# Kernel tuning notes

Measured on AMD Instinct MI355X. Metric: run time of the kernel, lower is better.

The kernel has to match this reference:

```python
import jax, jax.numpy as jnp
import numpy as np

N_NODES = 50000
N_EDGES = 1600000
HID = 256
NODE_F = 2
EDGE_F = 7
NUM_LAYERS = 3
EPS = 0.0  # GINEConv default eps


def _glorot(key, shape):
    fan_in, fan_out = shape[0], shape[1]
    lim = float(np.sqrt(6.0 / (fan_in + fan_out)))
    return jax.random.uniform(key, shape, jnp.float32, -lim, lim)


def setup_inputs() -> dict:
    key = jax.random.key(0)
    ks = jax.random.split(key, 16)
    x = jax.random.normal(ks[0], (N_NODES, NODE_F), jnp.float32)
    edge_index = jax.random.randint(ks[1], (2, N_EDGES), 0, N_NODES, jnp.int64)
    edge_attr = jax.random.normal(ks[2], (N_EDGES, EDGE_F), jnp.float32)
    # conv1: lin_edge1 (7->2), nn1 Linear(2->HID)
    We1 = _glorot(ks[3], (EDGE_F, NODE_F)); be1 = jnp.zeros((NODE_F,), jnp.float32)
    W1 = _glorot(ks[4], (NODE_F, HID));     b1 = jnp.zeros((HID,), jnp.float32)
    # conv2: lin_edge2 (7->HID), nn2 Linear(HID->HID)
    We2 = _glorot(ks[5], (EDGE_F, HID));    be2 = jnp.zeros((HID,), jnp.float32)
    W2 = _glorot(ks[6], (HID, HID));        b2 = jnp.zeros((HID,), jnp.float32)
    # endLinear HID->1
    Wend = _glorot(ks[7], (HID, 1));        bend = jnp.zeros((1,), jnp.float32)
    return dict(x=x, edge_index=edge_index, edge_attr=edge_attr,
                We1=We1, be1=be1, W1=W1, b1=b1,
                We2=We2, be2=be2, W2=W2, b2=b2,
                Wend=Wend, bend=bend)


def _gine_conv(h, src, dst, edge_emb, W, b):
    # message: relu(h[src] + lin_edge(edge_attr)); aggregate: scatter-sum at dst
    msg = jax.nn.relu(h[src] + edge_emb)                      # [E, C]
    aggr = jax.ops.segment_sum(msg, dst, num_segments=N_NODES)  # [N, C]
    return ((1.0 + EPS) * h + aggr) @ W + b                   # nn(...)


def reference(x, edge_index, edge_attr, We1, be1, W1, b1, We2, be2, W2, b2, Wend, bend):
    src, dst = edge_index[0], edge_index[1]
    # layer 1
    h = _gine_conv(x, src, dst, edge_attr @ We1 + be1, W1, b1)
    # layers 2..num_layers (shared conv2 weights, batchnorm disabled)
    edge_emb2 = edge_attr @ We2 + be2
    for _ in range(NUM_LAYERS - 1):
        h = jax.nn.relu(h)
        h = _gine_conv(h, src, dst, edge_emb2, W2, b2)
    h = jax.nn.relu(h)
    return jax.nn.sigmoid(h @ Wend + bend)  # [N, 1]
```

## Files before the change

kernel.cpp:

```cpp
#include <hip/hip_runtime.h>
#include <hip/hip_fp16.h>
#include <math.h>

#define N_NODES 50000
#define N_EDGES 1600000
#define HID 256
#define SCAN_B 196

typedef _Float16 f16x8 __attribute__((ext_vector_type(8)));
typedef float f32x4 __attribute__((ext_vector_type(4)));
typedef float v2f __attribute__((ext_vector_type(2)));

static __device__ __forceinline__ __half2 pk_max2(__half2 a, __half2 b) {
    unsigned au = *reinterpret_cast<unsigned*>(&a);
    unsigned bu = *reinterpret_cast<unsigned*>(&b);
    unsigned r;
    asm("v_pk_max_f16 %0, %1, %2" : "=v"(r) : "v"(au), "v"(bu));
    return *reinterpret_cast<__half2*>(&r);
}

static __device__ __forceinline__ unsigned h2u(float lo, float hi) {
    __half2 t = __floats2half2_rn(lo, hi);
    return *reinterpret_cast<unsigned*>(&t);
}

#define PKFMA_LO(ACC, ATTR, W)                                           \
    asm("v_pk_fma_f16 %0, %1, %2, %0 op_sel:[0,0,0] op_sel_hi:[0,1,1]"   \
        : "+v"(ACC) : "v"(ATTR), "v"(W))
#define PKFMA_HI(ACC, ATTR, W)                                           \
    asm("v_pk_fma_f16 %0, %1, %2, %0 op_sel:[1,0,0] op_sel_hi:[1,1,1]"   \
        : "+v"(ACC) : "v"(ATTR), "v"(W))

static __device__ __forceinline__ unsigned pack4_fp8(float a, float b, float c, float d) {
    int v = __builtin_amdgcn_cvt_pk_fp8_f32(a, b, 0, false);
    v = __builtin_amdgcn_cvt_pk_fp8_f32(c, d, v, true);
    return (unsigned)v;
}

__global__ __launch_bounds__(256) void hist_kernel(const int* __restrict__ dst,
                                                   int* __restrict__ deg) {
    const int T = gridDim.x * 256;
    const int t = blockIdx.x * 256 + threadIdx.x;
#pragma unroll
    for (int i = 0; i < 4; ++i) {
        int e = t + i * T;
        if (e < N_EDGES) atomicAdd(&deg[dst[e]], 1);
    }
}

__global__ __launch_bounds__(256) void scan1_kernel(const int* __restrict__ deg,
                                                    int* __restrict__ bsum) {
    int idx = blockIdx.x * 256 + threadIdx.x;
    int v = (idx < N_NODES) ? deg[idx] : 0;
#pragma unroll
    for (int off = 32; off > 0; off >>= 1) v += __shfl_down(v, off);
    __shared__ int ws[4];
    if ((threadIdx.x & 63) == 0) ws[threadIdx.x >> 6] = v;
    __syncthreads();
    if (threadIdx.x == 0) bsum[blockIdx.x] = ws[0] + ws[1] + ws[2] + ws[3];
}

__global__ __launch_bounds__(256) void scan2_kernel(int* __restrict__ bsum) {
    __shared__ int s[256];
    int t = threadIdx.x;
    int v = (t < SCAN_B) ? bsum[t] : 0;
    s[t] = v;
    __syncthreads();
    for (int off = 1; off < 256; off <<= 1) {
        int u = (t >= off) ? s[t - off] : 0;
        __syncthreads();
        s[t] += u;
        __syncthreads();
    }
    if (t < SCAN_B) bsum[t] = s[t] - v;
}

__global__ __launch_bounds__(256) void scan3_kernel(const int* __restrict__ deg,
                                                    const int* __restrict__ bsum,
                                                    int* __restrict__ base,
                                                    int* __restrict__ cursor) {
    __shared__ int s[256];
    int t = threadIdx.x;
    int idx = blockIdx.x * 256 + t;
    int v = (idx < N_NODES) ? deg[idx] : 0;
    s[t] = v;
    __syncthreads();
    for (int off = 1; off < 256; off <<= 1) {
        int u = (t >= off) ? s[t - off] : 0;
        __syncthreads();
        s[t] += u;
        __syncthreads();
    }
    if (idx < N_NODES) {
        int bv = bsum[blockIdx.x] + s[t] - v;
        base[idx] = bv;
        cursor[idx] = bv;
    }
    if (idx == 0) base[N_NODES] = N_EDGES;
}

static __device__ __forceinline__ void write_rec(float* __restrict__ rec, int pos,
                                                 const float* __restrict__ ep, int s) {
    float4 v;
    *(__half2*)&v.x = __floats2half2_rn(ep[0], ep[1]);
    *(__half2*)&v.y = __floats2half2_rn(ep[2], ep[3]);
    *(__half2*)&v.z = __floats2half2_rn(ep[4], ep[5]);
    unsigned w = (unsigned)__half_as_ushort(__float2half_rn(ep[6])) |
                 ((unsigned)s << 16);
    v.w = __uint_as_float(w);
    *(float4*)(rec + (size_t)pos * 4) = v;
}

__global__ __launch_bounds__(256) void scatter_rec_kernel(
        const int* __restrict__ src,
        const int* __restrict__ dst,
        const float* __restrict__ ea,
        int* __restrict__ cursor,
        float* __restrict__ rec) {
    const int T = gridDim.x * 256;
    const int t = blockIdx.x * 256 + threadIdx.x;
    const int e0 = t, e1 = t + T, e2 = t + 2 * T, e3 = t + 3 * T;
    const bool v3 = (e3 < N_EDGES);
    int d0 = dst[e0], d1 = dst[e1], d2 = dst[e2];
    int s0 = src[e0], s1 = src[e1], s2 = src[e2];
    int d3 = v3 ? dst[e3] : 0;
    int s3 = v3 ? src[e3] : 0;
    int p0 = atomicAdd(&cursor[d0], 1);
    int p1 = atomicAdd(&cursor[d1], 1);
    int p2 = atomicAdd(&cursor[d2], 1);
    int p3 = v3 ? atomicAdd(&cursor[d3], 1) : 0;
    write_rec(rec, p0, ea + (size_t)e0 * 7, s0);
    write_rec(rec, p1, ea + (size_t)e1 * 7, s1);
    write_rec(rec, p2, ea + (size_t)e2 * 7, s2);
    if (v3) write_rec(rec, p3, ea + (size_t)e3 * 7, s3);
}

__global__ __launch_bounds__(256) void layer1_kernel(
        const float* __restrict__ x,
        const float* __restrict__ rec,
        const int* __restrict__ base,
        const float* __restrict__ We1,
        const float* __restrict__ be1,
        const float* __restrict__ W1,
        const float* __restrict__ b1,
        unsigned* __restrict__ h8) {
    const int lane = threadIdx.x & 63;
    const int wid = threadIdx.x >> 6;
    const int n = blockIdx.x * 4 + wid;
    if (n >= N_NODES) return;
    float w00 = We1[0],  w01 = We1[1],  w10 = We1[2],  w11 = We1[3];
    float w20 = We1[4],  w21 = We1[5],  w30 = We1[6],  w31 = We1[7];
    float w40 = We1[8],  w41 = We1[9],  w50 = We1[10], w51 = We1[11];
    float w60 = We1[12], w61 = We1[13];
    float bb0 = be1[0], bb1 = be1[1];
    float m0 = 0.f, m1 = 0.f;
    const int s0 = base[n], s1 = base[n + 1];
    for (int pos = s0 + lane; pos < s1; pos += 64) {
        float4 a = *(const float4*)(rec + (size_t)pos * 4);
        __half2 hx = *(__half2*)&a.x;
        __half2 hy = *(__half2*)&a.y;
        __half2 hz = *(__half2*)&a.z;
        __half2 hw = *(__half2*)&a.w;
        unsigned uw = __float_as_uint(a.w);
        int s = (int)(uw >> 16);
        float a0 = __low2float(hx),  a1 = __high2float(hx);
        float a2 = __low2float(hy),  a3 = __high2float(hy);
        float a4 = __low2float(hz),  a5 = __high2float(hz);
        float a6 = __low2float(hw);
        float t0 = bb0, t1 = bb1;
        t0 = fmaf(a0, w00, t0); t1 = fmaf(a0, w01, t1);
        t0 = fmaf(a1, w10, t0); t1 = fmaf(a1, w11, t1);
        t0 = fmaf(a2, w20, t0); t1 = fmaf(a2, w21, t1);
        t0 = fmaf(a3, w30, t0); t1 = fmaf(a3, w31, t1);
        t0 = fmaf(a4, w40, t0); t1 = fmaf(a4, w41, t1);
        t0 = fmaf(a5, w50, t0); t1 = fmaf(a5, w51, t1);
        t0 = fmaf(a6, w60, t0); t1 = fmaf(a6, w61, t1);
        float2 xv = *(const float2*)&x[(size_t)s * 2];
        m0 += fmaxf(t0 + xv.x, 0.f);
        m1 += fmaxf(t1 + xv.y, 0.f);
    }
#pragma unroll
    for (int off = 32; off > 0; off >>= 1) {
        m0 += __shfl_down(m0, off);
        m1 += __shfl_down(m1, off);
    }
    m0 = __shfl(m0, 0);
    m1 = __shfl(m1, 0);
    const float t0 = x[n * 2 + 0] + m0;
    const float t1 = x[n * 2 + 1] + m1;
    const int c = lane * 4;
    float4 wa = *(const float4*)&W1[c];
    float4 wb = *(const float4*)&W1[256 + c];
    float4 bv = *(const float4*)&b1[c];
    float4 r;
    r.x = fmaxf(fmaf(t0, wa.x, fmaf(t1, wb.x, bv.x)), 0.f);
    r.y = fmaxf(fmaf(t0, wa.y, fmaf(t1, wb.y, bv.y)), 0.f);
    r.z = fmaxf(fmaf(t0, wa.z, fmaf(t1, wb.z, bv.z)), 0.f);
    r.w = fmaxf(fmaf(t0, wa.w, fmaf(t1, wb.w, bv.w)), 0.f);
    h8[(size_t)n * 64 + lane] = pack4_fp8(r.x, r.y, r.z, r.w);
}

#define EDGEH(RA, HU)                                                  \
    do {                                                               \
        unsigned _ux = __float_as_uint(RA.x);                          \
        unsigned _uy = __float_as_uint(RA.y);                          \
        unsigned _uz = __float_as_uint(RA.z);                          \
        unsigned _uw = __float_as_uint(RA.w);                          \
        unsigned _m0 = bb01u, _m1 = bb23u;                             \
        PKFMA_LO(_m0, _ux, w0au); PKFMA_LO(_m1, _ux, w0bu);            \
        PKFMA_HI(_m0, _ux, w1au); PKFMA_HI(_m1, _ux, w1bu);            \
        PKFMA_LO(_m0, _uy, w2au); PKFMA_LO(_m1, _uy, w2bu);            \
        PKFMA_HI(_m0, _uy, w3au); PKFMA_HI(_m1, _uy, w3bu);            \
        PKFMA_LO(_m0, _uz, w4au); PKFMA_LO(_m1, _uz, w4bu);            \
        PKFMA_HI(_m0, _uz, w5au); PKFMA_HI(_m1, _uz, w5bu);            \
        PKFMA_LO(_m0, _uw, w6au); PKFMA_LO(_m1, _uw, w6bu);            \
        v2f _hf0 = __builtin_amdgcn_cvt_pk_f32_fp8((int)(HU), false);  \
        v2f _hf1 = __builtin_amdgcn_cvt_pk_f32_fp8((int)(HU), true);   \
        __half2 _h0 = __float22half2_rn(make_float2(_hf0.x, _hf0.y));  \
        __half2 _h1 = __float22half2_rn(make_float2(_hf1.x, _hf1.y));  \
        __half2 _m0h = *reinterpret_cast<__half2*>(&_m0);              \
        __half2 _m1h = *reinterpret_cast<__half2*>(&_m1);              \
        _m0h = pk_max2(__hadd2(_m0h, _h0), z2);                        \
        _m1h = pk_max2(__hadd2(_m1h, _h1), z2);                        \
        acc0 = __hadd2(acc0, _m0h);                                    \
        acc1 = __hadd2(acc1, _m1h);                                    \
    } while (0)

#define HLOAD(RA) (h8[(size_t)((unsigned)__builtin_amdgcn_readfirstlane(       \
                       __float_as_int(RA.w)) >> 16) * 64 + lane])

#define LOADG(A0, A1, A2, A3, H0, H1, H2, H3, G)                       \
    do {                                                               \
        const float4* _p = rp + (size_t)(G) * 4;                       \
        A0 = _p[0]; A1 = _p[1]; A2 = _p[2]; A3 = _p[3];                \
        H0 = HLOAD(A0); H1 = HLOAD(A1);                                \
        H2 = HLOAD(A2); H3 = HLOAD(A3);                                \
    } while (0)

#define CONS4(A0, A1, A2, A3, H0, H1, H2, H3)                          \
    do {                                                               \
        EDGEH(A0, H0); EDGEH(A1, H1);                                  \
        EDGEH(A2, H2); EDGEH(A3, H3);                                  \
    } while (0)

__global__ __launch_bounds__(256) void aggr2_kernel(
        const unsigned* __restrict__ h8,
        const float* __restrict__ rec,
        const int* __restrict__ base,
        const float* __restrict__ We2,
        const float* __restrict__ be2,
        __half* __restrict__ accum) {
    const int lane = threadIdx.x & 63;
    const int n = blockIdx.x * 4 + (threadIdx.x >> 6);
    if (n >= N_NODES) return;
    const int c4 = lane * 4;
    const unsigned w0au = h2u(We2[0 * HID + c4], We2[0 * HID + c4 + 1]);
    const unsigned w0bu = h2u(We2[0 * HID + c4 + 2], We2[0 * HID + c4 + 3]);
    const unsigned w1au = h2u(We2[1 * HID + c4], We2[1 * HID + c4 + 1]);
    const unsigned w1bu = h2u(We2[1 * HID + c4 + 2], We2[1 * HID + c4 + 3]);
    const unsigned w2au = h2u(We2[2 * HID + c4], We2[2 * HID + c4 + 1]);
    const unsigned w2bu = h2u(We2[2 * HID + c4 + 2], We2[2 * HID + c4 + 3]);
    const unsigned w3au = h2u(We2[3 * HID + c4], We2[3 * HID + c4 + 1]);
    const unsigned w3bu = h2u(We2[3 * HID + c4 + 2], We2[3 * HID + c4 + 3]);
    const unsigned w4au = h2u(We2[4 * HID + c4], We2[4 * HID + c4 + 1]);
    const unsigned w4bu = h2u(We2[4 * HID + c4 + 2], We2[4 * HID + c4 + 3]);
    const unsigned w5au = h2u(We2[5 * HID + c4], We2[5 * HID + c4 + 1]);
    const unsigned w5bu = h2u(We2[5 * HID + c4 + 2], We2[5 * HID + c4 + 3]);
    const unsigned w6au = h2u(We2[6 * HID + c4], We2[6 * HID + c4 + 1]);
    const unsigned w6bu = h2u(We2[6 * HID + c4 + 2], We2[6 * HID + c4 + 3]);
    const unsigned bb01u = h2u(be2[c4], be2[c4 + 1]);
    const unsigned bb23u = h2u(be2[c4 + 2], be2[c4 + 3]);
    const __half2 z2 = __float2half2_rn(0.f);

    __half2 acc0, acc1;
    {
        unsigned hv = h8[(size_t)n * 64 + lane];
        v2f f0 = __builtin_amdgcn_cvt_pk_f32_fp8((int)hv, false);
        v2f f1 = __builtin_amdgcn_cvt_pk_f32_fp8((int)hv, true);
        acc0 = __float22half2_rn(make_float2(f0.x, f0.y));
        acc1 = __float22half2_rn(make_float2(f1.x, f1.y));
    }
    const int s0 = __builtin_amdgcn_readfirstlane(base[n]);
    const int deg = __builtin_amdgcn_readfirstlane(base[n + 1]) - s0;
    const float4* rp = (const float4*)rec + (size_t)s0;
    const int ng = deg >> 2;

    float4 r0, r1, r2, r3;
    unsigned rh0, rh1, rh2, rh3;
    float4 t0, t1, t2, t3;
    unsigned th0, th1, th2, th3;

    if (ng > 0) {
        LOADG(r0, r1, r2, r3, rh0, rh1, rh2, rh3, 0);
        int g = 1;
        for (; g + 1 < ng; g += 2) {
            LOADG(t0, t1, t2, t3, th0, th1, th2, th3, g);
            CONS4(r0, r1, r2, r3, rh0, rh1, rh2, rh3);
            LOADG(r0, r1, r2, r3, rh0, rh1, rh2, rh3, g + 1);
            CONS4(t0, t1, t2, t3, th0, th1, th2, th3);
        }
        if (g < ng) {
            LOADG(t0, t1, t2, t3, th0, th1, th2, th3, g);
            CONS4(r0, r1, r2, r3, rh0, rh1, rh2, rh3);
            CONS4(t0, t1, t2, t3, th0, th1, th2, th3);
        } else {
            CONS4(r0, r1, r2, r3, rh0, rh1, rh2, rh3);
        }
    }
    for (int i = ng * 4; i < deg; ++i) {
        float4 ra = rp[(size_t)i];
        unsigned hv = HLOAD(ra);
        EDGEH(ra, hv);
    }
    float2 of;
    *(__half2*)&of.x = acc0;
    *(__half2*)&of.y = acc1;
    *(float2*)&accum[(size_t)n * HID + c4] = of;
}

__global__ __launch_bounds__(256) void w2_swizzle_kernel(const float* __restrict__ W,
                                                         __half* __restrict__ W2s) {
    int t = blockIdx.x * 256 + threadIdx.x;
    if (t >= 16 * 8 * 64) return;
    int lane = t & 63;
    int kc = (t >> 6) & 7;
    int ct = t >> 9;
    int k0 = kc * 32 + (lane >> 4) * 8;
    int col = ct * 16 + (lane & 15);
#pragma unroll
    for (int j = 0; j < 8; ++j)
        W2s[(size_t)t * 8 + j] = __float2half(W[(size_t)(k0 + j) * HID + col]);
}

template <bool FUSE_END>
__global__ __launch_bounds__(256) void node2_mfma_kernel(
        const __half* __restrict__ A,
        const __half* __restrict__ W2s,
        const float* __restrict__ b,
        unsigned char* __restrict__ h8,
        const float* __restrict__ Wend,
        const float* __restrict__ bend,
        float* __restrict__ out) {
    const int lane = threadIdx.x & 63;
    const int wv = threadIdx.x >> 6;
    const int n_base = blockIdx.x * 64 + wv * 16;
    if (n_base >= N_NODES) return;
    const int quad = lane >> 4;
    const int mrow = lane & 15;
    f16x8 af[8];
    const __half* ap = A + (size_t)(n_base + mrow) * HID + quad * 8;
#pragma unroll
    for (int kc = 0; kc < 8; ++kc)
        af[kc] = *(const f16x8*)(ap + kc * 32);
    float p0 = 0.f, p1 = 0.f, p2 = 0.f, p3 = 0.f;
#pragma unroll
    for (int ct = 0; ct < 16; ++ct) {
        f32x4 c = {0.f, 0.f, 0.f, 0.f};
        const f16x8* bp = (const f16x8*)W2s + (size_t)(ct * 8) * 64 + lane;
#pragma unroll
        for (int kc = 0; kc < 8; ++kc)
            c = __builtin_amdgcn_mfma_f32_16x16x32_f16(af[kc], bp[(size_t)kc * 64],
                                                       c, 0, 0, 0);
        const int col = ct * 16 + mrow;
        const float bias = b[col];
        if (!FUSE_END) {
#pragma unroll
            for (int r = 0; r < 4; ++r) {
                int n = n_base + quad * 4 + r;
                float v = fmaxf(c[r] + bias, 0.f);
                int pk = __builtin_amdgcn_cvt_pk_fp8_f32(v, v, 0, false);
                if (n < N_NODES)
                    h8[(size_t)n * HID + col] = (unsigned char)(pk & 0xff);
            }
        } else {
            const float we = Wend[col];
            p0 = fmaf(fmaxf(c[0] + bias, 0.f), we, p0);
            p1 = fmaf(fmaxf(c[1] + bias, 0.f), we, p1);
            p2 = fmaf(fmaxf(c[2] + bias, 0.f), we, p2);
            p3 = fmaf(fmaxf(c[3] + bias, 0.f), we, p3);
        }
    }
    if (FUSE_END) {
#pragma unroll
        for (int mask = 1; mask < 16; mask <<= 1) {
            p0 += __shfl_xor(p0, mask);
            p1 += __shfl_xor(p1, mask);
            p2 += __shfl_xor(p2, mask);
            p3 += __shfl_xor(p3, mask);
        }
        if (mrow == 0) {
            const float bd = bend[0];
            int n = n_base + quad * 4;
            if (n + 0 < N_NODES) out[n + 0] = 1.f / (1.f + expf(-(p0 + bd)));
            if (n + 1 < N_NODES) out[n + 1] = 1.f / (1.f + expf(-(p1 + bd)));
            if (n + 2 < N_NODES) out[n + 2] = 1.f / (1.f + expf(-(p2 + bd)));
            if (n + 3 < N_NODES) out[n + 3] = 1.f / (1.f + expf(-(p3 + bd)));
        }
    }
}

extern "C" void kernel_launch(void* const* d_in, const int* in_sizes, int n_in,
                              void* d_out, int out_size, void* d_ws, size_t ws_size,
                              hipStream_t stream) {
    const float* x    = (const float*)d_in[0];
    const int*   ei   = (const int*)d_in[1];
    const float* ea   = (const float*)d_in[2];
    const float* We1  = (const float*)d_in[3];
    const float* be1  = (const float*)d_in[4];
    const float* W1   = (const float*)d_in[5];
    const float* b1   = (const float*)d_in[6];
    const float* We2  = (const float*)d_in[7];
    const float* be2  = (const float*)d_in[8];
    const float* W2   = (const float*)d_in[9];
    const float* b2   = (const float*)d_in[10];
    const float* Wend = (const float*)d_in[11];
    const float* bend = (const float*)d_in[12];
    float* out = (float*)d_out;

    const int* src = ei;
    const int* dst = ei + N_EDGES;

    const size_t HN = (size_t)N_NODES * HID;
    __half*   Bh   = (__half*)d_ws;
    unsigned* Ah   = (unsigned*)(Bh + HN);
    float*    rec  = (float*)(Ah + (size_t)N_NODES * 64);
    __half*   W2s  = (__half*)(rec + (size_t)N_EDGES * 4);
    int*   deg    = (int*)(W2s + 16 * 8 * 64 * 8);
    int*   cursor = deg + N_NODES;
    int*   base   = cursor + N_NODES;
    int*   bsum   = base + N_NODES + 2;

    const int E4_B = (N_EDGES + 4 * 256 - 1) / (4 * 256);

    hipMemsetAsync(deg, 0, (size_t)N_NODES * sizeof(int), stream);
    hist_kernel<<<E4_B, 256, 0, stream>>>(dst, deg);
    scan1_kernel<<<SCAN_B, 256, 0, stream>>>(deg, bsum);
    scan2_kernel<<<1, 256, 0, stream>>>(bsum);
    scan3_kernel<<<SCAN_B, 256, 0, stream>>>(deg, bsum, base, cursor);
    scatter_rec_kernel<<<E4_B, 256, 0, stream>>>(src, dst, ea, cursor, rec);
    w2_swizzle_kernel<<<32, 256, 0, stream>>>(W2, W2s);

    layer1_kernel<<<(N_NODES + 3) / 4, 256, 0, stream>>>(x, rec, base, We1, be1,
                                                         W1, b1, Ah);

    const int N2_B = (N_NODES + 63) / 64;
    aggr2_kernel<<<(N_NODES + 3) / 4, 256, 0, stream>>>(Ah, rec, base, We2, be2, Bh);
    node2_mfma_kernel<false><<<N2_B, 256, 0, stream>>>(Bh, W2s, b2,
                                                       (unsigned char*)Ah,
                                                       nullptr, nullptr, nullptr);
    aggr2_kernel<<<(N_NODES + 3) / 4, 256, 0, stream>>>(Ah, rec, base, We2, be2, Bh);
    node2_mfma_kernel<true><<<N2_B, 256, 0, stream>>>(Bh, W2s, b2, nullptr,
                                                      Wend, bend, out);
}
```

Measured before the change: 567.4 us.

## Split aggregation into channel passes with lanes processing four edges in parallel

The aggregation kernel now launches four passes over node blocks, each covering 64 of the 256 channels. Within a wave, 16 lanes cover channels and 4 lane groups take different edges, and partial sums are combined with xor shuffles. This replaces the serial per-edge loop in which all 64 lanes shared one edge, and adds nontemporal loads and stores. In exchange, edge records are read four times, only one quarter of the lanes store, and the gather h8 loads become per-lane (non-uniform) with masked tail edges.

Result: slower. 733.4 us (+29.3%).

```diff
diff --git a/kernel.cpp b/kernel.cpp
--- a/kernel.cpp
+++ b/kernel.cpp
@@ -6,6 +6,8 @@
 #define N_EDGES 1600000
 #define HID 256
 #define SCAN_B 196
+#define NPASS 4
+#define NB_PER_PASS ((N_NODES + 3) / 4)
 
 typedef _Float16 f16x8 __attribute__((ext_vector_type(8)));
 typedef float f32x4 __attribute__((ext_vector_type(4)));
@@ -22,6 +24,12 @@
 static __device__ __forceinline__ unsigned h2u(float lo, float hi) {
     __half2 t = __floats2half2_rn(lo, hi);
     return *reinterpret_cast<unsigned*>(&t);
+}
+
+static __device__ __forceinline__ __half2 shflx_h2(__half2 v, int m) {
+    int iv = *reinterpret_cast<int*>(&v);
+    iv = __shfl_xor(iv, m);
+    return *reinterpret_cast<__half2*>(&iv);
 }
 
 #define PKFMA_LO(ACC, ATTR, W)                                           \
@@ -200,7 +208,7 @@
     h8[(size_t)n * 64 + lane] = pack4_fp8(r.x, r.y, r.z, r.w);
 }
 
-#define EDGEH(RA, HU)                                                  \
+#define EDGEH4(RA, HU, VLD)                                            \
     do {                                                               \
         unsigned _ux = __float_as_uint(RA.x);                          \
         unsigned _uy = __float_as_uint(RA.y);                          \
@@ -222,25 +230,22 @@
         __half2 _m1h = *reinterpret_cast<__half2*>(&_m1);              \
         _m0h = pk_max2(__hadd2(_m0h, _h0), z2);                        \
         _m1h = pk_max2(__hadd2(_m1h, _h1), z2);                        \
-        acc0 = __hadd2(acc0, _m0h);                                    \
-        acc1 = __hadd2(acc1, _m1h);                                    \
+        unsigned _r0 = *reinterpret_cast<unsigned*>(&_m0h);            \
+        unsigned _r1 = *reinterpret_cast<unsigned*>(&_m1h);            \
+        _r0 = (VLD) ? _r0 : 0u;    \
+        _r1 = (VLD) ? _r1 : 0u;                                        \
+        acc0 = __hadd2(acc0, *reinterpret_cast<__half2*>(&_r0));       \
+        acc1 = __hadd2(acc1, *reinterpret_cast<__half2*>(&_r1));       \
     } while (0)
 
-#define HLOAD(RA) (h8[(size_t)((unsigned)__builtin_amdgcn_readfirstlane(       \
-                       __float_as_int(RA.w)) >> 16) * 64 + lane])
-
-#define LOADG(A0, A1, A2, A3, H0, H1, H2, H3, G)                       \
+#define LOADE(I, A, H, V)                                              \
     do {                                                               \
-        const float4* _p = rp + (size_t)(G) * 4;                       \
-        A0 = _p[0]; A1 = _p[1]; A2 = _p[2]; A3 = _p[3];                \
-        H0 = HLOAD(A0); H1 = HLOAD(A1);                                \
-        H2 = HLOAD(A2); H3 = HLOAD(A3);                                \
-    } while (0)
-
-#define CONS4(A0, A1, A2, A3, H0, H1, H2, H3)                          \
-    do {                                                               \
-        EDGEH(A0, H0); EDGEH(A1, H1);                                  \
-        EDGEH(A2, H2); EDGEH(A3, H3);                                  \
+        int _o = ((I) << 2) + es;                                      \
+        V = _o < deg;                                                  \
+        int _oc = V ? _o : (deg - 1);                                  \
+        A = __builtin_nontemporal_load(rbase + _oc);                   \
+        unsigned _s = __float_as_uint(A.w) >> 16;                      \
+        H = h8[(size_t)_s * 64 + cd];                                  \
     } while (0)
 
 __global__ __launch_bounds__(256) void aggr2_kernel(
@@ -251,9 +256,14 @@
         const float* __restrict__ be2,
         __half* __restrict__ accum) {
     const int lane = threadIdx.x & 63;
-    const int n = blockIdx.x * 4 + (threadIdx.x >> 6);
+    const int pass = blockIdx.x / NB_PER_PASS;
+    const int nb   = blockIdx.x - pass * NB_PER_PASS;
+    const int n = nb * 4 + (threadIdx.x >> 6);
     if (n >= N_NODES) return;
-    const int c4 = lane * 4;
+    const int c  = lane & 15;
+    const int es = lane >> 4;
+    const int cd = pass * 16 + c;
+    const int c4 = cd * 4;
     const unsigned w0au = h2u(We2[0 * HID + c4], We2[0 * HID + c4 + 1]);
     const unsigned w0bu = h2u(We2[0 * HID + c4 + 2], We2[0 * HID + c4 + 3]);
     const unsigned w1au = h2u(We2[1 * HID + c4], We2[1 * HID + c4 + 1]);
@@ -272,50 +282,47 @@
     const unsigned bb23u = h2u(be2[c4 + 2], be2[c4 + 3]);
     const __half2 z2 = __float2half2_rn(0.f);
 
-    __half2 acc0, acc1;
-    {
-        unsigned hv = h8[(size_t)n * 64 + lane];
+    const int s0  = __builtin_amdgcn_readfirstlane(base[n]);
+    const int deg = __builtin_amdgcn_readfirstlane(base[n + 1]) - s0;
+    const f32x4* rbase = (const f32x4*)rec + (size_t)s0;
+
+    __half2 acc0 = z2, acc1 = z2;
+    const int nIter = (deg + 3) >> 2;
+    if (nIter > 0) {
+        f32x4 a0; unsigned h0; bool v0;
+        LOADE(0, a0, h0, v0);
+        int i = 1;
+        for (; i + 1 < nIter; i += 2) {
+            f32x4 a1; unsigned h1; bool v1;
+            LOADE(i, a1, h1, v1);
+            EDGEH4(a0, h0, v0);
+            LOADE(i + 1, a0, h0, v0);
+            EDGEH4(a1, h1, v1);
+        }
+        if (i < nIter) {
+            f32x4 a1; unsigned h1; bool v1;
+            LOADE(i, a1, h1, v1);
+            EDGEH4(a0, h0, v0);
+            EDGEH4(a1, h1, v1);
+        } else {
+            EDGEH4(a0, h0, v0);
+        }
+    }
+    acc0 = __hadd2(acc0, shflx_h2(acc0, 16));
+    acc0 = __hadd2(acc0, shflx_h2(acc0, 32));
+    acc1 = __hadd2(acc1, shflx_h2(acc1, 16));
+    acc1 = __hadd2(acc1, shflx_h2(acc1, 32));
+    if (es == 0) {
+        unsigned hv = h8[(size_t)n * 64 + cd];
         v2f f0 = __builtin_amdgcn_cvt_pk_f32_fp8((int)hv, false);
         v2f f1 = __builtin_amdgcn_cvt_pk_f32_fp8((int)hv, true);
-        acc0 = __float22half2_rn(make_float2(f0.x, f0.y));
-        acc1 = __float22half2_rn(make_float2(f1.x, f1.y));
-    }
-    const int s0 = __builtin_amdgcn_readfirstlane(base[n]);
-    const int deg = __builtin_amdgcn_readfirstlane(base[n + 1]) - s0;
-    const float4* rp = (const float4*)rec + (size_t)s0;
-    const int ng = deg >> 2;
-
-    float4 r0, r1, r2, r3;
-    unsigned rh0, rh1, rh2, rh3;
-    float4 t0, t1, t2, t3;
-    unsigned th0, th1, th2, th3;
-
-    if (ng > 0) {
-        LOADG(r0, r1, r2, r3, rh0, rh1, rh2, rh3, 0);
-        int g = 1;
-        for (; g + 1 < ng; g += 2) {
-            LOADG(t0, t1, t2, t3, th0, th1, th2, th3, g);
-            CONS4(r0, r1, r2, r3, rh0, rh1, rh2, rh3);
-            LOADG(r0, r1, r2, r3, rh0, rh1, rh2, rh3, g + 1);
-            CONS4(t0, t1, t2, t3, th0, th1, th2, th3);
-        }
-        if (g < ng) {
-            LOADG(t0, t1, t2, t3, th0, th1, th2, th3, g);
-            CONS4(r0, r1, r2, r3, rh0, rh1, rh2, rh3);
-            CONS4(t0, t1, t2, t3, th0, th1, th2, th3);
-        } else {
-            CONS4(r0, r1, r2, r3, rh0, rh1, rh2, rh3);
-        }
-    }
-    for (int i = ng * 4; i < deg; ++i) {
-        float4 ra = rp[(size_t)i];
-        unsigned hv = HLOAD(ra);
-        EDGEH(ra, hv);
-    }
-    float2 of;
-    *(__half2*)&of.x = acc0;
-    *(__half2*)&of.y = acc1;
-    *(float2*)&accum[(size_t)n * HID + c4] = of;
+        acc0 = __hadd2(acc0, __float22half2_rn(make_float2(f0.x, f0.y)));
+        acc1 = __hadd2(acc1, __float22half2_rn(make_float2(f1.x, f1.y)));
+        v2f of;
+        of.x = *reinterpret_cast<float*>(&acc0);
+        of.y = *reinterpret_cast<float*>(&acc1);
+        __builtin_nontemporal_store(of, (v2f*)(accum + (size_t)n * HID + c4));
+    }
 }
 
 __global__ __launch_bounds__(256) void w2_swizzle_kernel(const float* __restrict__ W,
@@ -444,11 +451,12 @@
                                                          W1, b1, Ah);
 
     const int N2_B = (N_NODES + 63) / 64;
-    aggr2_kernel<<<(N_NODES + 3) / 4, 256, 0, stream>>>(Ah, rec, base, We2, be2, Bh);
+    const int AG_B = NPASS * NB_PER_PASS;
+    aggr2_kernel<<<AG_B, 256, 0, stream>>>(Ah, rec, base, We2, be2, Bh);
     node2_mfma_kernel<false><<<N2_B, 256, 0, stream>>>(Bh, W2s, b2,
                                                        (unsigned char*)Ah,
                                                        nullptr, nullptr, nullptr);
-    aggr2_kernel<<<(N_NODES + 3) / 4, 256, 0, stream>>>(Ah, rec, base, We2, be2, Bh);
+    aggr2_kernel<<<AG_B, 256, 0, stream>>>(Ah, rec, base, We2, be2, Bh);
     node2_mfma_kernel<true><<<N2_B, 256, 0, stream>>>(Bh, W2s, b2, nullptr,
                                                       Wend, bend, out);
 }
```

## Bin CSR edges by source range and process bins in lockstep for gather locality

Applied to the files above, without the earlier changes.

Sorts edges within each destination by one of 8 source-id bins. Each workgroup then sweeps its 128 nodes bin by bin, accumulating partial sums in LDS, so that concurrent h8 gathers hit a narrow source range and reuse cache better. The price is 8x larger histogram, scan and cursor arrays, plus a multi-chunk scan. The aggregation loop also loses its software prefetch pipelining, adds per-bin overhead and fp16 partial accumulation, and launches far fewer workgroups.

Measured after the change: 1.126 ms. 98.5% more time.

```diff
diff --git a/kernel.cpp b/kernel.cpp
--- a/kernel.cpp
+++ b/kernel.cpp
@@ -5,7 +5,12 @@
 #define N_NODES 50000
 #define N_EDGES 1600000
 #define HID 256
-#define SCAN_B 196
+#define NBIN 8
+#define BINW 6250
+#define M2 (N_NODES * NBIN)
+#define SB2 ((M2 + 255) / 256)
+#define V2_NODES 128
+#define V2_GRID ((N_NODES + V2_NODES - 1) / V2_NODES)
 
 typedef _Float16 f16x8 __attribute__((ext_vector_type(8)));
 typedef float f32x4 __attribute__((ext_vector_type(4)));
@@ -24,6 +29,13 @@
     return *reinterpret_cast<unsigned*>(&t);
 }
 
+static __device__ __forceinline__ __half2 u2h(unsigned u) {
+    return *reinterpret_cast<__half2*>(&u);
+}
+static __device__ __forceinline__ unsigned h2bits(__half2 h) {
+    return *reinterpret_cast<unsigned*>(&h);
+}
+
 #define PKFMA_LO(ACC, ATTR, W)                                           \
     asm("v_pk_fma_f16 %0, %1, %2, %0 op_sel:[0,0,0] op_sel_hi:[0,1,1]"   \
         : "+v"(ACC) : "v"(ATTR), "v"(W))
@@ -37,21 +49,25 @@
     return (unsigned)v;
 }
 
-__global__ __launch_bounds__(256) void hist_kernel(const int* __restrict__ dst,
-                                                   int* __restrict__ deg) {
+__global__ __launch_bounds__(256) void hist_kernel(const int* __restrict__ src,
+                                                   const int* __restrict__ dst,
+                                                   int* __restrict__ deg2) {
     const int T = gridDim.x * 256;
     const int t = blockIdx.x * 256 + threadIdx.x;
 #pragma unroll
     for (int i = 0; i < 4; ++i) {
         int e = t + i * T;
-        if (e < N_EDGES) atomicAdd(&deg[dst[e]], 1);
-    }
-}
-
-__global__ __launch_bounds__(256) void scan1_kernel(const int* __restrict__ deg,
+        if (e < N_EDGES) {
+            int d = dst[e], s = src[e];
+            atomicAdd(&deg2[d * NBIN + s / BINW], 1);
+        }
+    }
+}
+
+__global__ __launch_bounds__(256) void scan1_kernel(const int* __restrict__ deg2,
                                                     int* __restrict__ bsum) {
     int idx = blockIdx.x * 256 + threadIdx.x;
-    int v = (idx < N_NODES) ? deg[idx] : 0;
+    int v = (idx < M2) ? deg2[idx] : 0;
 #pragma unroll
     for (int off = 32; off > 0; off >>= 1) v += __shfl_down(v, off);
     __shared__ int ws[4];
@@ -62,8 +78,40 @@
 
 __global__ __launch_bounds__(256) void scan2_kernel(int* __restrict__ bsum) {
     __shared__ int s[256];
+    __shared__ int carry_s;
     int t = threadIdx.x;
-    int v = (t < SCAN_B) ? bsum[t] : 0;
+    if (t == 0) carry_s = 0;
+    __syncthreads();
+    const int NCH = (SB2 + 255) / 256;
+    for (int c = 0; c < NCH; ++c) {
+        int idx = c * 256 + t;
+        int v = (idx < SB2) ? bsum[idx] : 0;
+        s[t] = v;
+        __syncthreads();
+        for (int off = 1; off < 256; off <<= 1) {
+            int u = (t >= off) ? s[t - off] : 0;
+            __syncthreads();
+            s[t] += u;
+            __syncthreads();
+        }
+        int incl = s[t];
+        int tot  = s[255];
+        int base = carry_s;
+        __syncthreads();
+        if (idx < SB2) bsum[idx] = base + incl - v;
+        if (t == 0) carry_s = base + tot;
+        __syncthreads();
+    }
+}
+
+__global__ __launch_bounds__(256) void scan3_kernel(const int* __restrict__ deg2,
+                                                    const int* __restrict__ bsum,
+                                                    int* __restrict__ base2,
+                                                    int* __restrict__ cursor2) {
+    __shared__ int s[256];
+    int t = threadIdx.x;
+    int idx = blockIdx.x * 256 + t;
+    int v = (idx < M2) ? deg2[idx] : 0;
     s[t] = v;
     __syncthreads();
     for (int off = 1; off < 256; off <<= 1) {
@@ -72,31 +120,12 @@
         s[t] += u;
         __syncthreads();
     }
-    if (t < SCAN_B) bsum[t] = s[t] - v;
-}
-
-__global__ __launch_bounds__(256) void scan3_kernel(const int* __restrict__ deg,
-                                                    const int* __restrict__ bsum,
-                                                    int* __restrict__ base,
-                                                    int* __restrict__ cursor) {
-    __shared__ int s[256];
-    int t = threadIdx.x;
-    int idx = blockIdx.x * 256 + t;
-    int v = (idx < N_NODES) ? deg[idx] : 0;
-    s[t] = v;
-    __syncthreads();
-    for (int off = 1; off < 256; off <<= 1) {
-        int u = (t >= off) ? s[t - off] : 0;
-        __syncthreads();
-        s[t] += u;
-        __syncthreads();
-    }
-    if (idx < N_NODES) {
+    if (idx < M2) {
         int bv = bsum[blockIdx.x] + s[t] - v;
-        base[idx] = bv;
-        cursor[idx] = bv;
-    }
-    if (idx == 0) base[N_NODES] = N_EDGES;
+        base2[idx] = bv;
+        cursor2[idx] = bv;
+    }
+    if (idx == 0) base2[M2] = N_EDGES;
 }
 
 static __device__ __forceinline__ void write_rec(float* __restrict__ rec, int pos,
@@ -115,7 +144,7 @@
         const int* __restrict__ src,
         const int* __restrict__ dst,
         const float* __restrict__ ea,
-        int* __restrict__ cursor,
+        int* __restrict__ cursor2,
         float* __restrict__ rec) {
     const int T = gridDim.x * 256;
     const int t = blockIdx.x * 256 + threadIdx.x;
@@ -125,10 +154,10 @@
     int s0 = src[e0], s1 = src[e1], s2 = src[e2];
     int d3 = v3 ? dst[e3] : 0;
     int s3 = v3 ? src[e3] : 0;
-    int p0 = atomicAdd(&cursor[d0], 1);
-    int p1 = atomicAdd(&cursor[d1], 1);
-    int p2 = atomicAdd(&cursor[d2], 1);
-    int p3 = v3 ? atomicAdd(&cursor[d3], 1) : 0;
+    int p0 = atomicAdd(&cursor2[d0 * NBIN + s0 / BINW], 1);
+    int p1 = atomicAdd(&cursor2[d1 * NBIN + s1 / BINW], 1);
+    int p2 = atomicAdd(&cursor2[d2 * NBIN + s2 / BINW], 1);
+    int p3 = v3 ? atomicAdd(&cursor2[d3 * NBIN + s3 / BINW], 1) : 0;
     write_rec(rec, p0, ea + (size_t)e0 * 7, s0);
     write_rec(rec, p1, ea + (size_t)e1 * 7, s1);
     write_rec(rec, p2, ea + (size_t)e2 * 7, s2);
@@ -138,7 +167,7 @@
 __global__ __launch_bounds__(256) void layer1_kernel(
         const float* __restrict__ x,
         const float* __restrict__ rec,
-        const int* __restrict__ base,
+        const int* __restrict__ base2,
         const float* __restrict__ We1,
         const float* __restrict__ be1,
         const float* __restrict__ W1,
@@ -154,7 +183,7 @@
     float w60 = We1[12], w61 = We1[13];
     float bb0 = be1[0], bb1 = be1[1];
     float m0 = 0.f, m1 = 0.f;
-    const int s0 = base[n], s1 = base[n + 1];
+    const int s0 = base2[n * NBIN], s1 = base2[n * NBIN + NBIN];
     for (int pos = s0 + lane; pos < s1; pos += 64) {
         float4 a = *(const float4*)(rec + (size_t)pos * 4);
         __half2 hx = *(__half2*)&a.x;
@@ -200,7 +229,7 @@
     h8[(size_t)n * 64 + lane] = pack4_fp8(r.x, r.y, r.z, r.w);
 }
 
-#define EDGEH(RA, HU)                                                  \
+#define EDGEH4(RA, HU, VLD)                                            \
     do {                                                               \
         unsigned _ux = __float_as_uint(RA.x);                          \
         unsigned _uy = __float_as_uint(RA.y);                          \
@@ -218,41 +247,27 @@
         v2f _hf1 = __builtin_amdgcn_cvt_pk_f32_fp8((int)(HU), true);   \
         __half2 _h0 = __float22half2_rn(make_float2(_hf0.x, _hf0.y));  \
         __half2 _h1 = __float22half2_rn(make_float2(_hf1.x, _hf1.y));  \
-        __half2 _m0h = *reinterpret_cast<__half2*>(&_m0);              \
-        __half2 _m1h = *reinterpret_cast<__half2*>(&_m1);              \
+        __half2 _m0h = u2h(_m0), _m1h = u2h(_m1);                      \
         _m0h = pk_max2(__hadd2(_m0h, _h0), z2);                        \
         _m1h = pk_max2(__hadd2(_m1h, _h1), z2);                        \
-        acc0 = __hadd2(acc0, _m0h);                                    \
-        acc1 = __hadd2(acc1, _m1h);                                    \
-    } while (0)
-
-#define HLOAD(RA) (h8[(size_t)((unsigned)__builtin_amdgcn_readfirstlane(       \
-                       __float_as_int(RA.w)) >> 16) * 64 + lane])
-
-#define LOADG(A0, A1, A2, A3, H0, H1, H2, H3, G)                       \
-    do {                                                               \
-        const float4* _p = rp + (size_t)(G) * 4;                       \
-        A0 = _p[0]; A1 = _p[1]; A2 = _p[2]; A3 = _p[3];                \
-        H0 = HLOAD(A0); H1 = HLOAD(A1);                                \
-        H2 = HLOAD(A2); H3 = HLOAD(A3);                                \
-    } while (0)
-
-#define CONS4(A0, A1, A2, A3, H0, H1, H2, H3)                          \
-    do {                                                               \
-        EDGEH(A0, H0); EDGEH(A1, H1);                                  \
-        EDGEH(A2, H2); EDGEH(A3, H3);                                  \
+        unsigned _r0 = h2bits(_m0h), _r1 = h2bits(_m1h);               \
+        _r0 = (VLD) ? _r0 : 0u;       \
+        _r1 = (VLD) ? _r1 : 0u;                                        \
+        acc0 = __hadd2(acc0, u2h(_r0));                                \
+        acc1 = __hadd2(acc1, u2h(_r1));                                \
     } while (0)
 
 __global__ __launch_bounds__(256) void aggr2_kernel(
         const unsigned* __restrict__ h8,
         const float* __restrict__ rec,
-        const int* __restrict__ base,
+        const int* __restrict__ base2,
         const float* __restrict__ We2,
         const float* __restrict__ be2,
         __half* __restrict__ accum) {
+    __shared__ uint2 accs[V2_NODES * 64];
     const int lane = threadIdx.x & 63;
-    const int n = blockIdx.x * 4 + (threadIdx.x >> 6);
-    if (n >= N_NODES) return;
+    const int w = threadIdx.x >> 6;
+    const int n0 = blockIdx.x * V2_NODES + w * 32;
     const int c4 = lane * 4;
     const unsigned w0au = h2u(We2[0 * HID + c4], We2[0 * HID + c4 + 1]);
     const unsigned w0bu = h2u(We2[0 * HID + c4 + 2], We2[0 * HID + c4 + 3]);
@@ -272,50 +287,53 @@
     const unsigned bb23u = h2u(be2[c4 + 2], be2[c4 + 3]);
     const __half2 z2 = __float2half2_rn(0.f);
 
-    __half2 acc0, acc1;
-    {
+    uint2* ap = accs + (size_t)(w * 32) * 64 + lane;
+    for (int j = 0; j < 32; ++j) ap[j * 64] = make_uint2(0u, 0u);
+
+    const f32x4* rp = (const f32x4*)rec;
+    for (int b = 0; b < NBIN; ++b) {
+        for (int j = 0; j < 32; ++j) {
+            int n = n0 + j;
+            if (n >= N_NODES) break;
+            int s0 = __builtin_amdgcn_readfirstlane(base2[n * NBIN + b]);
+            int s1 = __builtin_amdgcn_readfirstlane(base2[n * NBIN + b + 1]);
+            if (s1 <= s0) continue;
+            __half2 acc0 = z2, acc1 = z2;
+            int last = s1 - 1;
+            for (int e = s0; e < s1; e += 4) {
+                int i1 = min(e + 1, last), i2 = min(e + 2, last), i3 = min(e + 3, last);
+                bool v1 = (e + 1 <= last), v2 = (e + 2 <= last), v3 = (e + 3 <= last);
+                f32x4 a0 = rp[e], a1 = rp[i1], a2 = rp[i2], a3 = rp[i3];
+                unsigned h0 = h8[(size_t)(__float_as_uint(a0.w) >> 16) * 64 + lane];
+                unsigned h1 = h8[(size_t)(__float_as_uint(a1.w) >> 16) * 64 + lane];
+                unsigned h2 = h8[(size_t)(__float_as_uint(a2.w) >> 16) * 64 + lane];
+                unsigned h3 = h8[(size_t)(__float_as_uint(a3.w) >> 16) * 64 + lane];
+                EDGEH4(a0, h0, true);
+                EDGEH4(a1, h1, v1);
+                EDGEH4(a2, h2, v2);
+                EDGEH4(a3, h3, v3);
+            }
+            uint2 p = ap[j * 64];
+            p.x = h2bits(__hadd2(u2h(p.x), acc0));
+            p.y = h2bits(__hadd2(u2h(p.y), acc1));
+            ap[j * 64] = p;
+        }
+    }
+    for (int j = 0; j < 32; ++j) {
+        int n = n0 + j;
+        if (n >= N_NODES) break;
+        uint2 p = ap[j * 64];
+        __half2 acc0 = u2h(p.x), acc1 = u2h(p.y);
         unsigned hv = h8[(size_t)n * 64 + lane];
         v2f f0 = __builtin_amdgcn_cvt_pk_f32_fp8((int)hv, false);
         v2f f1 = __builtin_amdgcn_cvt_pk_f32_fp8((int)hv, true);
-        acc0 = __float22half2_rn(make_float2(f0.x, f0.y));
-        acc1 = __float22half2_rn(make_float2(f1.x, f1.y));
-    }
-    const int s0 = __builtin_amdgcn_readfirstlane(base[n]);
-    const int deg = __builtin_amdgcn_readfirstlane(base[n + 1]) - s0;
-    const float4* rp = (const float4*)rec + (size_t)s0;
-    const int ng = deg >> 2;
-
-    float4 r0, r1, r2, r3;
-    unsigned rh0, rh1, rh2, rh3;
-    float4 t0, t1, t2, t3;
-    unsigned th0, th1, th2, th3;
-
-    if (ng > 0) {
-        LOADG(r0, r1, r2, r3, rh0, rh1, rh2, rh3, 0);
-        int g = 1;
-        for (; g + 1 < ng; g += 2) {
-            LOADG(t0, t1, t2, t3, th0, th1, th2, th3, g);
-            CONS4(r0, r1, r2, r3, rh0, rh1, rh2, rh3);
-            LOADG(r0, r1, r2, r3, rh0, rh1, rh2, rh3, g + 1);
-            CONS4(t0, t1, t2, t3, th0, th1, th2, th3);
-        }
-        if (g < ng) {
-            LOADG(t0, t1, t2, t3, th0, th1, th2, th3, g);
-            CONS4(r0, r1, r2, r3, rh0, rh1, rh2, rh3);
-            CONS4(t0, t1, t2, t3, th0, th1, th2, th3);
-        } else {
-            CONS4(r0, r1, r2, r3, rh0, rh1, rh2, rh3);
-        }
-    }
-    for (int i = ng * 4; i < deg; ++i) {
-        float4 ra = rp[(size_t)i];
-        unsigned hv = HLOAD(ra);
-        EDGEH(ra, hv);
-    }
-    float2 of;
-    *(__half2*)&of.x = acc0;
-    *(__half2*)&of.y = acc1;
-    *(float2*)&accum[(size_t)n * HID + c4] = of;
+        acc0 = __hadd2(acc0, __float22half2_rn(make_float2(f0.x, f0.y)));
+        acc1 = __hadd2(acc1, __float22half2_rn(make_float2(f1.x, f1.y)));
+        float2 of;
+        *(__half2*)&of.x = acc0;
+        *(__half2*)&of.y = acc1;
+        *(float2*)&accum[(size_t)n * HID + c4] = of;
+    }
 }
 
 __global__ __launch_bounds__(256) void w2_swizzle_kernel(const float* __restrict__ W,
@@ -425,30 +443,30 @@
     unsigned* Ah   = (unsigned*)(Bh + HN);
     float*    rec  = (float*)(Ah + (size_t)N_NODES * 64);
     __half*   W2s  = (__half*)(rec + (size_t)N_EDGES * 4);
-    int*   deg    = (int*)(W2s + 16 * 8 * 64 * 8);
-    int*   cursor = deg + N_NODES;
-    int*   base   = cursor + N_NODES;
-    int*   bsum   = base + N_NODES + 2;
+    int*   deg2    = (int*)(W2s + 16 * 8 * 64 * 8);
+    int*   cursor2 = deg2 + M2;
+    int*   base2   = cursor2 + M2;
+    int*   bsum    = base2 + M2 + 1;
 
     const int E4_B = (N_EDGES + 4 * 256 - 1) / (4 * 256);
 
-    hipMemsetAsync(deg, 0, (size_t)N_NODES * sizeof(int), stream);
-    hist_kernel<<<E4_B, 256, 0, stream>>>(dst, deg);
-    scan1_kernel<<<SCAN_B, 256, 0, stream>>>(deg, bsum);
+    hipMemsetAsync(deg2, 0, (size_t)M2 * sizeof(int), stream);
+    hist_kernel<<<E4_B, 256, 0, stream>>>(src, dst, deg2);
+    scan1_kernel<<<SB2, 256, 0, stream>>>(deg2, bsum);
     scan2_kernel<<<1, 256, 0, stream>>>(bsum);
-    scan3_kernel<<<SCAN_B, 256, 0, stream>>>(deg, bsum, base, cursor);
-    scatter_rec_kernel<<<E4_B, 256, 0, stream>>>(src, dst, ea, cursor, rec);
+    scan3_kernel<<<SB2, 256, 0, stream>>>(deg2, bsum, base2, cursor2);
+    scatter_rec_kernel<<<E4_B, 256, 0, stream>>>(src, dst, ea, cursor2, rec);
     w2_swizzle_kernel<<<32, 256, 0, stream>>>(W2, W2s);
 
-    layer1_kernel<<<(N_NODES + 3) / 4, 256, 0, stream>>>(x, rec, base, We1, be1,
+    layer1_kernel<<<(N_NODES + 3) / 4, 256, 0, stream>>>(x, rec, base2, We1, be1,
                                                          W1, b1, Ah);
 
     const int N2_B = (N_NODES + 63) / 64;
-    aggr2_kernel<<<(N_NODES + 3) / 4, 256, 0, stream>>>(Ah, rec, base, We2, be2, Bh);
+    aggr2_kernel<<<V2_GRID, 256, 0, stream>>>(Ah, rec, base2, We2, be2, Bh);
     node2_mfma_kernel<false><<<N2_B, 256, 0, stream>>>(Bh, W2s, b2,
                                                        (unsigned char*)Ah,
                                                        nullptr, nullptr, nullptr);
-    aggr2_kernel<<<(N_NODES + 3) / 4, 256, 0, stream>>>(Ah, rec, base, We2, be2, Bh);
+    aggr2_kernel<<<V2_GRID, 256, 0, stream>>>(Ah, rec, base2, We2, be2, Bh);
     node2_mfma_kernel<true><<<N2_B, 256, 0, stream>>>(Bh, W2s, b2, nullptr,
                                                       Wend, bend, out);
 }
```
